# Kernel tuning notes

Measured on AMD Instinct MI355X. Metric: run time of the kernel, lower is better.

The kernel has to match this reference:

```python
import jax, jax.numpy as jnp
import numpy as np

# geometry constants from init_kwargs
VX, VY, VZ = 0.1, 0.1, 4.0
X_OFF, Y_OFF, Z_OFF = VX / 2 - 51.2, VY / 2 - 51.2, VZ / 2 - 3.0
GY, GX = 1024, 1024  # round((51.2-(-51.2))/0.1)
NUM_BEV = 8
BN_EPS = 1e-3


def setup_inputs() -> dict:
    key = jax.random.key(0)
    k1, k2, k3, k4, k5, k6 = jax.random.split(key, 6)
    N, P, C_in, C_out = 40000, 32, 10, 64
    voxel_features = jax.random.normal(k1, (N, P, 4), jnp.float32)
    voxel_num_points = jax.random.randint(k2, (N,), 1, P + 1, jnp.int32)
    bb = jax.random.randint(k3, (N,), 0, 2, jnp.int32)
    yy = jax.random.randint(k4, (N,), 0, GY, jnp.int32)
    xx = jax.random.randint(k5, (N,), 0, GX, jnp.int32)
    coords = jnp.stack([bb, jnp.zeros((N,), jnp.int32), yy, xx], axis=1)
    record_len = jnp.array([N // 2, N - N // 2], jnp.int32)
    W = jax.random.normal(k6, (C_in, C_out), jnp.float32) * 0.1
    gamma = jnp.ones((C_out,), jnp.float32)
    beta = jnp.zeros((C_out,), jnp.float32)
    run_mean = jnp.zeros((C_out,), jnp.float32)
    run_var = jnp.ones((C_out,), jnp.float32)
    return {"voxel_features": voxel_features, "W": W, "gamma": gamma,
            "beta": beta, "run_mean": run_mean, "run_var": run_var,
            "voxel_num_points": voxel_num_points, "coords": coords,
            "record_len": record_len}


def reference(voxel_features, W, gamma, beta, run_mean, run_var,
              voxel_num_points, coords, record_len):
    N, P, _ = voxel_features.shape
    npts = voxel_num_points.astype(voxel_features.dtype)  # [N]
    xyz = voxel_features[:, :, :3]

    # cluster offset feature
    points_mean = xyz.sum(axis=1, keepdims=True) / npts[:, None, None]
    f_cluster = xyz - points_mean

    # pillar-center offset feature
    cx = coords[:, 3].astype(voxel_features.dtype)[:, None] * VX + X_OFF
    cy = coords[:, 2].astype(voxel_features.dtype)[:, None] * VY + Y_OFF
    cz = coords[:, 1].astype(voxel_features.dtype)[:, None] * VZ + Z_OFF
    f_center = jnp.stack([xyz[:, :, 0] - cx, xyz[:, :, 1] - cy,
                          xyz[:, :, 2] - cz], axis=-1)

    features = jnp.concatenate([voxel_features, f_cluster, f_center], axis=-1)  # [N,P,10]

    # padding mask
    mask = (voxel_num_points[:, None] > jnp.arange(P, dtype=jnp.int32)[None, :])
    mask = mask[..., None].astype(voxel_features.dtype)  # [N,P,1]
    features = features * mask

    # PFN layer: Linear(10->64, no bias) + BN(eval) + ReLU + max over points
    x = jnp.einsum('npc,cd->npd', features, W)  # [N,P,64]
    x = (x - run_mean) * jax.lax.rsqrt(run_var + BN_EPS) * gamma + beta
    x = jax.nn.relu(x)
    pillar_features = x.max(axis=1)  # [N,64]

    # hand-crafted BEV stats
    safe_n = jnp.clip(npts, 1.0)[:, None]  # [N,1]
    num_points_norm = npts[:, None] / P
    intensity = voxel_features[:, :, 3:4]
    mean_intensity = (intensity * mask).sum(axis=1) / safe_n
    z = xyz[:, :, 2:3]
    mean_height = (z * mask).sum(axis=1) / safe_n
    max_height = (z * mask + (1 - mask) * -1e6).max(axis=1)
    min_height = (z * mask + (1 - mask) * 1e6).min(axis=1)
    height_span = max_height - min_height
    pm = (xyz * mask).sum(axis=1, keepdims=True) / safe_n[:, :, None]
    var_xyz = (((xyz - pm) ** 2) * mask).sum(axis=1) / safe_n  # [N,3]
    pillar_bev = jnp.concatenate([num_points_norm, mean_intensity, mean_height,
                                  max_height, height_span, var_xyz[:, 0:1],
                                  var_xyz[:, 1:2], var_xyz[:, 2:3]], axis=1)  # [N,8]

    batch_size = record_len.shape[0]
    b = jnp.clip(coords[:, 0], 0, batch_size - 1)
    y_idx = coords[:, 2]
    x_idx = coords[:, 3]
    vox_bev = jnp.zeros((batch_size, NUM_BEV, GY, GX), voxel_features.dtype)
    vox_bev = vox_bev.at[b, :, y_idx, x_idx].set(pillar_bev)

    return pillar_features, vox_bev
```

## Files before the change

kernel.cpp:

```cpp
#include <hip/hip_runtime.h>

#define GYD 1024
#define GXD 1024
#define NUM_BEV 8

__device__ __forceinline__ float rdlane(float x, int l) {
    return __int_as_float(__builtin_amdgcn_readlane(__float_as_int(x), l));
}
__device__ __forceinline__ float rsum32(float x) {
#pragma unroll
    for (int o = 1; o < 32; o <<= 1) x += __shfl_xor(x, o, 64);
    return x;
}
__device__ __forceinline__ float rmax32(float x) {
#pragma unroll
    for (int o = 1; o < 32; o <<= 1) x = fmaxf(x, __shfl_xor(x, o, 64));
    return x;
}
__device__ __forceinline__ float rmin32(float x) {
#pragma unroll
    for (int o = 1; o < 32; o <<= 1) x = fminf(x, __shfl_xor(x, o, 64));
    return x;
}

__global__ __launch_bounds__(256) void pillar_kernel(
    const float4* __restrict__ vf,
    const float* __restrict__ W,
    const float* __restrict__ gammap, const float* __restrict__ betap,
    const float* __restrict__ rmeanp, const float* __restrict__ rvarp,
    const int* __restrict__ npts_arr,
    const int* __restrict__ coords,
    float* __restrict__ pillar_out,
    float* __restrict__ bev_vals,
    int* __restrict__ winner,
    int N, int bs)
{
    __shared__ float4 pts[4][2][32];
    const int wid  = threadIdx.x >> 6;
    const int lane = threadIdx.x & 63;
    const int half = lane >> 5;
    const int sl   = lane & 31;
    const int n0   = blockIdx.x * 8 + wid * 2;
    const int n    = n0 + half;
    const bool valid = (n < N);
    const int nn = valid ? n : 0;

    const int d = lane;
    const float w0 = W[d],       w1 = W[64 + d],  w2 = W[128 + d], w3 = W[192 + d];
    const float w4 = W[256 + d], w5 = W[320 + d], w6 = W[384 + d];
    const float w7 = W[448 + d], w8 = W[512 + d], w9 = W[576 + d];
    const float g  = gammap[d], bt = betap[d], rm = rmeanp[d], rv = rvarp[d];

    const int npts = npts_arr[nn];
    const int4 crd = ((const int4*)coords)[nn];
    const float cx = (float)crd.w * 0.1f - 51.15f;
    const float cy = (float)crd.z * 0.1f - 51.15f;
    const float cz = (float)crd.y * 4.0f - 1.0f;

    float4 v = make_float4(0.f, 0.f, 0.f, 0.f);
    if (valid) v = vf[(size_t)nn * 32 + sl];
    const bool pv = sl < npts;
    const int src = half << 5;
    float4 v0;
    v0.x = __shfl(v.x, src, 64); v0.y = __shfl(v.y, src, 64);
    v0.z = __shfl(v.z, src, 64); v0.w = __shfl(v.w, src, 64);
    pts[wid][half][sl] = pv ? v : v0;

    const float m = pv ? 1.f : 0.f;
    const float sx   = rsum32(v.x);
    const float sy   = rsum32(v.y);
    const float sz   = rsum32(v.z);
    const float smx  = rsum32(v.x * m);
    const float smy  = rsum32(v.y * m);
    const float smz  = rsum32(v.z * m);
    const float smI  = rsum32(v.w * m);
    const float sx2  = rsum32(v.x * v.x * m);
    const float sy2  = rsum32(v.y * v.y * m);
    const float sz2  = rsum32(v.z * v.z * m);
    const float maxz = rmax32(pv ? v.z : -1e6f);
    const float minz = rmin32(pv ? v.z :  1e6f);

    __syncthreads();

    const float scale = g * rsqrtf(rv + 1e-3f);
    const float shift = fmaf(-rm, scale, bt);
    const float A = (w0 + w4 + w7) * scale;
    const float B = (w1 + w5 + w8) * scale;
    const float C = (w2 + w6 + w9) * scale;
    const float D = w3 * scale;

#pragma unroll
    for (int h = 0; h < 2; ++h) {
        const int L  = h << 5;
        const int nh = __builtin_amdgcn_readlane(npts, L);
        const float invnh = 1.f / (float)nh;
        const float mx = rdlane(sx, L) * invnh, my = rdlane(sy, L) * invnh, mz = rdlane(sz, L) * invnh;
        const float cxh = rdlane(cx, L), cyh = rdlane(cy, L), czh = rdlane(cz, L);
        const float E   = -(mx * w4 + my * w5 + mz * w6 + cxh * w7 + cyh * w8 + czh * w9);
        const float bse = fmaf(E, scale, shift);

        float a0 = -1e30f, a1 = -1e30f, a2 = -1e30f, a3 = -1e30f;
#pragma unroll
        for (int p = 0; p < 32; p += 4) {
            const float4 q0 = pts[wid][h][p + 0];
            const float4 q1 = pts[wid][h][p + 1];
            const float4 q2 = pts[wid][h][p + 2];
            const float4 q3 = pts[wid][h][p + 3];
            a0 = fmaxf(a0, fmaf(q0.x, A, fmaf(q0.y, B, fmaf(q0.z, C, fmaf(q0.w, D, bse)))));
            a1 = fmaxf(a1, fmaf(q1.x, A, fmaf(q1.y, B, fmaf(q1.z, C, fmaf(q1.w, D, bse)))));
            a2 = fmaxf(a2, fmaf(q2.x, A, fmaf(q2.y, B, fmaf(q2.z, C, fmaf(q2.w, D, bse)))));
            a3 = fmaxf(a3, fmaf(q3.x, A, fmaf(q3.y, B, fmaf(q3.z, C, fmaf(q3.w, D, bse)))));
        }
        float acc = fmaxf(fmaxf(a0, a1), fmaxf(a2, a3));
        if (nh < 32) acc = fmaxf(acc, shift);
        acc = fmaxf(acc, 0.f);
        const int np_ = n0 + h;
        if (np_ < N) pillar_out[(size_t)np_ * 64 + lane] = acc;
    }

    if (valid && sl == 0) {
        const float fn = (float)npts, invn = 1.f / fn;
        const float pmx = smx * invn, pmy = smy * invn, pmz = smz * invn;
        const float vvx = fmaf(-pmx, pmx, sx2 * invn);
        const float vvy = fmaf(-pmy, pmy, sy2 * invn);
        const float vvz = fmaf(-pmz, pmz, sz2 * invn);
        float4* bvp = (float4*)&bev_vals[(size_t)n * 8];
        bvp[0] = make_float4(fn * (1.f / 32.f), smI * invn, pmz, maxz);
        bvp[1] = make_float4(maxz - minz, vvx, vvy, vvz);
        const int b = crd.x < 0 ? 0 : (crd.x > bs - 1 ? bs - 1 : crd.x);
        atomicMax(&winner[(b * GYD + crd.z) * GXD + crd.w], n + 1);
    }
}

__global__ __launch_bounds__(256) void bev_fill(
    const int* __restrict__ winner,
    const float* __restrict__ bev_vals,
    float* __restrict__ vox_bev, int bs)
{
    const int cell = blockIdx.x * 256 + threadIdx.x;
    const int w = winner[cell];
    float4 lo = make_float4(0.f, 0.f, 0.f, 0.f), hi = lo;
    if (w > 0) {
        const float4* bvp = (const float4*)&bev_vals[(size_t)(w - 1) * 8];
        lo = bvp[0]; hi = bvp[1];
    }
    const int b  = cell >> 20;
    const int yx = cell & ((1 << 20) - 1);
    float* basep = vox_bev + (((size_t)b * NUM_BEV) << 20) + yx;
    basep[(size_t)0 << 20] = lo.x; basep[(size_t)1 << 20] = lo.y;
    basep[(size_t)2 << 20] = lo.z; basep[(size_t)3 << 20] = lo.w;
    basep[(size_t)4 << 20] = hi.x; basep[(size_t)5 << 20] = hi.y;
    basep[(size_t)6 << 20] = hi.z; basep[(size_t)7 << 20] = hi.w;
}

extern "C" void kernel_launch(void* const* d_in, const int* in_sizes, int n_in,
                              void* d_out, int out_size, void* d_ws, size_t ws_size,
                              hipStream_t stream) {
    const float4* vf    = (const float4*)d_in[0];
    const float* W      = (const float*)d_in[1];
    const float* gammap = (const float*)d_in[2];
    const float* betap  = (const float*)d_in[3];
    const float* rmeanp = (const float*)d_in[4];
    const float* rvarp  = (const float*)d_in[5];
    const int* npts     = (const int*)d_in[6];
    const int* coords   = (const int*)d_in[7];
    const int N  = in_sizes[6];
    const int bs = in_sizes[8];

    float* pillar_out = (float*)d_out;
    float* vox_bev    = (float*)d_out + (size_t)N * 64;

    int* winner     = (int*)d_ws;
    float* bev_vals = (float*)((char*)d_ws + (size_t)bs * GYD * GXD * sizeof(int));

    hipMemsetAsync(winner, 0, (size_t)bs * GYD * GXD * sizeof(int), stream);

    const int blocksA = (N + 7) / 8;
    pillar_kernel<<<blocksA, 256, 0, stream>>>(vf, W, gammap, betap, rmeanp, rvarp,
                                               npts, coords, pillar_out, bev_vals,
                                               winner, N, bs);
    const int blocksB = (bs << 20) / 256;
    bev_fill<<<blocksB, 256, 0, stream>>>(winner, bev_vals, vox_bev, bs);
}
```

Baseline: 135.9 us.

## Use DPP reductions, register-broadcast points, and vectorize BEV fill by four cells

Cross-lane reductions now use DPP row operations in place of shuffles. The pillar max loop reads points straight from registers through readlane and stops at the real point count, so the shared-memory staging and the block barrier go away. The BEV fill kernel handles four cells per thread with int4 winner loads and float4 stores, and takes a fast path that writes zeros when all four cells are empty. The readlane loop has a data-dependent trip count, which serializes work per point, and the DPP reduction correctness depends on the row_bcast semantics.

```diff
diff --git a/kernel.cpp b/kernel.cpp
--- a/kernel.cpp
+++ b/kernel.cpp
@@ -4,22 +4,36 @@
 #define GXD 1024
 #define NUM_BEV 8
 
-__device__ __forceinline__ float rdlane(float x, int l) {
+__device__ __forceinline__ float rdlanef(float x, int l) {
     return __int_as_float(__builtin_amdgcn_readlane(__float_as_int(x), l));
 }
-__device__ __forceinline__ float rsum32(float x) {
-#pragma unroll
-    for (int o = 1; o < 32; o <<= 1) x += __shfl_xor(x, o, 64);
+template <int CTRL, int ROWMASK>
+__device__ __forceinline__ float dppf(float x, float oldv) {
+    return __int_as_float(__builtin_amdgcn_update_dpp(
+        __float_as_int(oldv), __float_as_int(x), CTRL, ROWMASK, 0xF, false));
+}
+__device__ __forceinline__ float dsum32(float x) {
+    x += dppf<0x111, 0xF>(x, 0.f);
+    x += dppf<0x112, 0xF>(x, 0.f);
+    x += dppf<0x114, 0xF>(x, 0.f);
+    x += dppf<0x118, 0xF>(x, 0.f);
+    x += dppf<0x142, 0xA>(x, 0.f);
     return x;
 }
-__device__ __forceinline__ float rmax32(float x) {
-#pragma unroll
-    for (int o = 1; o < 32; o <<= 1) x = fmaxf(x, __shfl_xor(x, o, 64));
+__device__ __forceinline__ float dmax32(float x) {
+    x = fmaxf(x, dppf<0x111, 0xF>(x, x));
+    x = fmaxf(x, dppf<0x112, 0xF>(x, x));
+    x = fmaxf(x, dppf<0x114, 0xF>(x, x));
+    x = fmaxf(x, dppf<0x118, 0xF>(x, x));
+    x = fmaxf(x, dppf<0x142, 0xA>(x, x));
     return x;
 }
-__device__ __forceinline__ float rmin32(float x) {
-#pragma unroll
-    for (int o = 1; o < 32; o <<= 1) x = fminf(x, __shfl_xor(x, o, 64));
+__device__ __forceinline__ float dmin32(float x) {
+    x = fminf(x, dppf<0x111, 0xF>(x, x));
+    x = fminf(x, dppf<0x112, 0xF>(x, x));
+    x = fminf(x, dppf<0x114, 0xF>(x, x));
+    x = fminf(x, dppf<0x118, 0xF>(x, x));
+    x = fminf(x, dppf<0x142, 0xA>(x, x));
     return x;
 }
 
@@ -35,7 +49,6 @@
     int* __restrict__ winner,
     int N, int bs)
 {
-    __shared__ float4 pts[4][2][32];
     const int wid  = threadIdx.x >> 6;
     const int lane = threadIdx.x & 63;
     const int half = lane >> 5;
@@ -60,27 +73,20 @@
     float4 v = make_float4(0.f, 0.f, 0.f, 0.f);
     if (valid) v = vf[(size_t)nn * 32 + sl];
     const bool pv = sl < npts;
-    const int src = half << 5;
-    float4 v0;
-    v0.x = __shfl(v.x, src, 64); v0.y = __shfl(v.y, src, 64);
-    v0.z = __shfl(v.z, src, 64); v0.w = __shfl(v.w, src, 64);
-    pts[wid][half][sl] = pv ? v : v0;
+    const float m = pv ? 1.f : 0.f;
 
-    const float m = pv ? 1.f : 0.f;
-    const float sx   = rsum32(v.x);
-    const float sy   = rsum32(v.y);
-    const float sz   = rsum32(v.z);
-    const float smx  = rsum32(v.x * m);
-    const float smy  = rsum32(v.y * m);
-    const float smz  = rsum32(v.z * m);
-    const float smI  = rsum32(v.w * m);
-    const float sx2  = rsum32(v.x * v.x * m);
-    const float sy2  = rsum32(v.y * v.y * m);
-    const float sz2  = rsum32(v.z * v.z * m);
-    const float maxz = rmax32(pv ? v.z : -1e6f);
-    const float minz = rmin32(pv ? v.z :  1e6f);
-
-    __syncthreads();
+    const float sx   = dsum32(v.x);
+    const float sy   = dsum32(v.y);
+    const float sz   = dsum32(v.z);
+    const float smx  = dsum32(v.x * m);
+    const float smy  = dsum32(v.y * m);
+    const float smz  = dsum32(v.z * m);
+    const float smI  = dsum32(v.w * m);
+    const float sx2  = dsum32(v.x * v.x * m);
+    const float sy2  = dsum32(v.y * v.y * m);
+    const float sz2  = dsum32(v.z * v.z * m);
+    const float maxz = dmax32(pv ? v.z : -1e6f);
+    const float minz = dmin32(pv ? v.z :  1e6f);
 
     const float scale = g * rsqrtf(rv + 1e-3f);
     const float shift = fmaf(-rm, scale, bt);
@@ -94,31 +100,28 @@
         const int L  = h << 5;
         const int nh = __builtin_amdgcn_readlane(npts, L);
         const float invnh = 1.f / (float)nh;
-        const float mx = rdlane(sx, L) * invnh, my = rdlane(sy, L) * invnh, mz = rdlane(sz, L) * invnh;
-        const float cxh = rdlane(cx, L), cyh = rdlane(cy, L), czh = rdlane(cz, L);
+        const float mx = rdlanef(sx, L + 31) * invnh;
+        const float my = rdlanef(sy, L + 31) * invnh;
+        const float mz = rdlanef(sz, L + 31) * invnh;
+        const float cxh = rdlanef(cx, L), cyh = rdlanef(cy, L), czh = rdlanef(cz, L);
         const float E   = -(mx * w4 + my * w5 + mz * w6 + cxh * w7 + cyh * w8 + czh * w9);
         const float bse = fmaf(E, scale, shift);
 
-        float a0 = -1e30f, a1 = -1e30f, a2 = -1e30f, a3 = -1e30f;
-#pragma unroll
-        for (int p = 0; p < 32; p += 4) {
-            const float4 q0 = pts[wid][h][p + 0];
-            const float4 q1 = pts[wid][h][p + 1];
-            const float4 q2 = pts[wid][h][p + 2];
-            const float4 q3 = pts[wid][h][p + 3];
-            a0 = fmaxf(a0, fmaf(q0.x, A, fmaf(q0.y, B, fmaf(q0.z, C, fmaf(q0.w, D, bse)))));
-            a1 = fmaxf(a1, fmaf(q1.x, A, fmaf(q1.y, B, fmaf(q1.z, C, fmaf(q1.w, D, bse)))));
-            a2 = fmaxf(a2, fmaf(q2.x, A, fmaf(q2.y, B, fmaf(q2.z, C, fmaf(q2.w, D, bse)))));
-            a3 = fmaxf(a3, fmaf(q3.x, A, fmaf(q3.y, B, fmaf(q3.z, C, fmaf(q3.w, D, bse)))));
+        float acc = -1e30f;
+        for (int p = 0; p < nh; ++p) {
+            const float qx = rdlanef(v.x, L + p);
+            const float qy = rdlanef(v.y, L + p);
+            const float qz = rdlanef(v.z, L + p);
+            const float qw = rdlanef(v.w, L + p);
+            acc = fmaxf(acc, fmaf(qx, A, fmaf(qy, B, fmaf(qz, C, fmaf(qw, D, bse)))));
         }
-        float acc = fmaxf(fmaxf(a0, a1), fmaxf(a2, a3));
         if (nh < 32) acc = fmaxf(acc, shift);
         acc = fmaxf(acc, 0.f);
         const int np_ = n0 + h;
         if (np_ < N) pillar_out[(size_t)np_ * 64 + lane] = acc;
     }
 
-    if (valid && sl == 0) {
+    if (valid && sl == 31) {
         const float fn = (float)npts, invn = 1.f / fn;
         const float pmx = smx * invn, pmy = smy * invn, pmz = smz * invn;
         const float vvx = fmaf(-pmx, pmx, sx2 * invn);
@@ -133,24 +136,32 @@
 }
 
 __global__ __launch_bounds__(256) void bev_fill(
-    const int* __restrict__ winner,
+    const int4* __restrict__ winner4,
     const float* __restrict__ bev_vals,
     float* __restrict__ vox_bev, int bs)
 {
-    const int cell = blockIdx.x * 256 + threadIdx.x;
-    const int w = winner[cell];
-    float4 lo = make_float4(0.f, 0.f, 0.f, 0.f), hi = lo;
-    if (w > 0) {
-        const float4* bvp = (const float4*)&bev_vals[(size_t)(w - 1) * 8];
-        lo = bvp[0]; hi = bvp[1];
+    const int gidx = blockIdx.x * 256 + threadIdx.x;
+    const int4 w = winner4[gidx];
+    const int c0 = gidx << 2;
+    const int b  = c0 >> 20;
+    const int yx = c0 & ((1 << 20) - 1);
+    float* basep = vox_bev + (((size_t)b * NUM_BEV) << 20) + yx;
+    if ((w.x | w.y | w.z | w.w) == 0) {
+        const float4 z4 = make_float4(0.f, 0.f, 0.f, 0.f);
+#pragma unroll
+        for (int k = 0; k < NUM_BEV; ++k)
+            *(float4*)(basep + ((size_t)k << 20)) = z4;
+    } else {
+#pragma unroll
+        for (int k = 0; k < NUM_BEV; ++k) {
+            float4 o;
+            o.x = (w.x > 0) ? bev_vals[(size_t)(w.x - 1) * 8 + k] : 0.f;
+            o.y = (w.y > 0) ? bev_vals[(size_t)(w.y - 1) * 8 + k] : 0.f;
+            o.z = (w.z > 0) ? bev_vals[(size_t)(w.z - 1) * 8 + k] : 0.f;
+            o.w = (w.w > 0) ? bev_vals[(size_t)(w.w - 1) * 8 + k] : 0.f;
+            *(float4*)(basep + ((size_t)k << 20)) = o;
+        }
     }
-    const int b  = cell >> 20;
-    const int yx = cell & ((1 << 20) - 1);
-    float* basep = vox_bev + (((size_t)b * NUM_BEV) << 20) + yx;
-    basep[(size_t)0 << 20] = lo.x; basep[(size_t)1 << 20] = lo.y;
-    basep[(size_t)2 << 20] = lo.z; basep[(size_t)3 << 20] = lo.w;
-    basep[(size_t)4 << 20] = hi.x; basep[(size_t)5 << 20] = hi.y;
-    basep[(size_t)6 << 20] = hi.z; basep[(size_t)7 << 20] = hi.w;
 }
 
 extern "C" void kernel_launch(void* const* d_in, const int* in_sizes, int n_in,
@@ -179,6 +190,6 @@
     pillar_kernel<<<blocksA, 256, 0, stream>>>(vf, W, gammap, betap, rmeanp, rvarp,
                                                npts, coords, pillar_out, bev_vals,
                                                winner, N, bs);
-    const int blocksB = (bs << 20) / 256;
-    bev_fill<<<blocksB, 256, 0, stream>>>(winner, bev_vals, vox_bev, bs);
+    const int blocksB = (bs << 20) / (256 * 4);
+    bev_fill<<<blocksB, 256, 0, stream>>>((const int4*)winner, bev_vals, vox_bev, bs);
 }
```

New measurement: 142.5 us. 1.05x slower.
